# Kernel optimization log

Hardware: AMD Instinct MI355X
Metric: run time of the kernel (lower is better)

Reference implementation:

```python
import jax, jax.numpy as jnp
import numpy as np
from jax import lax

IMAGE_SIZE = 512
N_REWEIGHT = 3
BLUR_RADIUS = 4  # GaussianBlur(4)
BLUR_SIGMA = 4.0


def _cdist(a, b):
    # Euclidean distance matrix [N, M] via ||a||^2 + ||b||^2 - 2 a.b
    a2 = jnp.sum(a * a, axis=1)[:, None]
    b2 = jnp.sum(b * b, axis=1)[None, :]
    d2 = a2 + b2 - 2.0 * (a @ b.T)
    return jnp.sqrt(jnp.maximum(d2, 0.0))


def _gaussian_blur(img):
    # separable depthwise gaussian blur, kernel size 2*radius+1, SAME padding
    x = jnp.arange(-BLUR_RADIUS, BLUR_RADIUS + 1, dtype=img.dtype)
    g = jnp.exp(-(x * x) / (2.0 * BLUR_SIGMA * BLUR_SIGMA))
    g = g / jnp.sum(g)
    dn = ('NCHW', 'OIHW', 'NCHW')
    img = lax.conv_general_dilated(img, g.reshape(1, 1, -1, 1), (1, 1), 'SAME', dimension_numbers=dn)
    img = lax.conv_general_dilated(img, g.reshape(1, 1, 1, -1), (1, 1), 'SAME', dimension_numbers=dn)
    return img


def setup_inputs() -> dict:
    key = jax.random.key(0)
    k1, k2 = jax.random.split(key)
    h, w, d, m = 64, 64, 384, 65536
    patch = jax.random.normal(k1, (h * w, d), dtype=jnp.float32)
    patch_lib = jax.random.normal(k2, (m, d), dtype=jnp.float32)
    return {"patch": patch, "patch_lib": patch_lib, "fmap_h": h, "fmap_w": w}


def reference(patch, patch_lib, fmap_h, fmap_w):
    # dist: [N, M] full pairwise cdist against coreset library
    dist = _cdist(patch, patch_lib)
    min_val = jnp.min(dist, axis=1)            # [N] NN distance per test patch
    min_idx = jnp.argmin(dist, axis=1)         # [N]
    s_idx = jnp.argmax(min_val)
    s_star = jnp.max(min_val)
    m_test = patch[s_idx]                      # [D]
    m_star = patch_lib[min_idx[s_idx]]         # [D]
    # w_dist = cdist(m_star, patch_lib): single-row distance
    w_dist = jnp.sqrt(jnp.maximum(jnp.sum((m_star[None, :] - patch_lib) ** 2, axis=1), 0.0))
    neg_top, nn_idx = lax.top_k(-w_dist, N_REWEIGHT)   # k smallest
    m_star_knn = jnp.linalg.norm(m_test[None, :] - patch_lib[nn_idx[1:]], axis=1)  # [k-1]
    D = jnp.sqrt(jnp.asarray(patch.shape[1], dtype=patch.dtype))
    w = 1.0 - jnp.exp(s_star / D) / jnp.sum(jnp.exp(m_star_knn / D))
    s = w * s_star
    s_map = min_val.reshape(1, 1, fmap_h, fmap_w)
    s_map = jax.image.resize(s_map, (1, 1, IMAGE_SIZE, IMAGE_SIZE), method='bilinear')
    s_map = _gaussian_blur(s_map)
    return s, s_map
```

## Files before the change

### kernel.cpp

```cpp
#include <hip/hip_runtime.h>

#define NP 4096
#define DIM 384
#define ML 65536

typedef int i32x4 __attribute__((ext_vector_type(4)));
typedef unsigned short u16;
typedef unsigned long long u64;

#define QSCALE 21.16666667f
#define B2SCALE 224.0138889f
#define KBIAS (1 << 23)

typedef __attribute__((address_space(1))) unsigned int as1_u32;
typedef __attribute__((address_space(3))) unsigned int as3_u32;

__device__ __forceinline__ void gl_lds16(const void* g, void* l) {
  __builtin_amdgcn_global_load_lds((const as1_u32*)g, (as3_u32*)l, 16, 0, 0);
}

__global__ __launch_bounds__(256) void prep_kernel(const float* __restrict__ patch,
                                                   const float* __restrict__ lib,
                                                   char* __restrict__ Ai8,
                                                   char* __restrict__ Bi8,
                                                   int* __restrict__ b2i) {
  const int row = blockIdx.x * 4 + (threadIdx.x >> 6);
  const int lane = threadIdx.x & 63;
  const float* src;
  char* dst;
  int r;
  if (row < NP) { src = patch; dst = Ai8; r = row; }
  else          { src = lib;   dst = Bi8; r = row - NP; }
  float s = 0.f;
#pragma unroll
  for (int j = 0; j < 3; ++j) {
    const float2 v = *reinterpret_cast<const float2*>(src + (size_t)r * DIM + j * 128 + lane * 2);
    s += v.x * v.x + v.y * v.y;
    const int q0 = __float2int_rn(fminf(fmaxf(v.x, -6.f), 6.f) * QSCALE);
    const int q1 = __float2int_rn(fminf(fmaxf(v.y, -6.f), 6.f) * QSCALE);
    const u16 p = (u16)((q0 & 0xFF) | ((q1 & 0xFF) << 8));
    *reinterpret_cast<u16*>(dst + (size_t)r * DIM + j * 128 + lane * 2) = p;
  }
#pragma unroll
  for (int m = 1; m < 64; m <<= 1) s += __shfl_xor(s, m);
  if (lane == 0 && row >= NP) b2i[r] = __float2int_rn(s * B2SCALE);
}

__global__ __launch_bounds__(512, 2) void gemm_min_kernel(const char* __restrict__ Ai8,
                                                          const char* __restrict__ Bi8,
                                                          const int* __restrict__ b2i,
                                                          u64* __restrict__ packed) {
  __shared__ __align__(16) char As[2][32768];
  __shared__ __align__(16) char Bs[2][32768];
  const int tid = threadIdx.x;
  const int lane = tid & 63;
  const int w = tid >> 6;
  const int wm = w >> 2;
  const int wn = w & 3;
  const int cl = lane & 15, rg = lane >> 4;

  const int orig = blockIdx.x;
  const int logical = (orig & 7) * 512 + (orig >> 3);
  const int xt = logical & 15;
  const int yt = logical >> 4;
  const int n0 = xt * 256;
  const int m0 = yt * 256;

  const char* ga[4]; const char* gb[4]; int lof[4];
#pragma unroll
  for (int i = 0; i < 4; ++i) {
    const int P = i * 8192 + tid * 16;
    const int r = P >> 7;
    const int L = P ^ ((r & 7) << 4);
    const int c = L & 127;
    lof[i] = P;
    ga[i] = Ai8 + (size_t)(n0 + r) * DIM + c;
    gb[i] = Bi8 + (size_t)(m0 + r) * DIM + c;
  }

  int offA[2][8], offB[2][4];
#pragma unroll
  for (int g = 0; g < 2; ++g) {
#pragma unroll
    for (int j = 0; j < 8; ++j) {
      const int row = wm * 128 + j * 16 + cl;
      offA[g][j] = row * 128 + ((g * 64 + rg * 16) ^ ((cl & 7) << 4));
    }
#pragma unroll
    for (int i = 0; i < 4; ++i) {
      const int row = wn * 64 + i * 16 + cl;
      offB[g][i] = row * 128 + ((g * 64 + rg * 16) ^ ((cl & 7) << 4));
    }
  }

  i32x4 acc[4][8] = {};

#pragma unroll
  for (int i = 0; i < 4; ++i) { gl_lds16(ga[i], (char*)As[0] + lof[i]); ga[i] += 128; }
#pragma unroll
  for (int i = 0; i < 4; ++i) { gl_lds16(gb[i], (char*)Bs[0] + lof[i]); gb[i] += 128; }

#pragma unroll
  for (int kt = 0; kt < 3; ++kt) {
    const int buf = kt & 1;
    if (kt < 2) {
#pragma unroll
      for (int i = 0; i < 4; ++i) { gl_lds16(ga[i], (char*)As[buf ^ 1] + lof[i]); ga[i] += 128; }
#pragma unroll
      for (int i = 0; i < 4; ++i) { gl_lds16(gb[i], (char*)Bs[buf ^ 1] + lof[i]); gb[i] += 128; }
      asm volatile("s_waitcnt vmcnt(8)" ::: "memory");
    } else {
      asm volatile("s_waitcnt vmcnt(0)" ::: "memory");
    }
    __builtin_amdgcn_s_barrier();
    __builtin_amdgcn_sched_barrier(0);

    const char* Ab = (const char*)As[buf];
    const char* Bb = (const char*)Bs[buf];
#pragma unroll
    for (int g = 0; g < 2; ++g) {
      i32x4 af[8], bg[4];
#pragma unroll
      for (int j = 0; j < 8; ++j)
        af[j] = *reinterpret_cast<const i32x4*>(Ab + offA[g][j]);
#pragma unroll
      for (int i = 0; i < 4; ++i)
        bg[i] = *reinterpret_cast<const i32x4*>(Bb + offB[g][i]);
#pragma unroll
      for (int i = 0; i < 4; ++i)
#pragma unroll
        for (int j = 0; j < 8; ++j)
          acc[i][j] = __builtin_amdgcn_mfma_i32_16x16x64_i8(bg[i], af[j], acc[i][j], 0, 0, 0);
    }
    __builtin_amdgcn_s_barrier();
    __builtin_amdgcn_sched_barrier(0);
  }

  const int colb = m0 + wn * 64 + rg * 4;
  i32x4 bc[4];
#pragma unroll
  for (int i = 0; i < 4; ++i)
    bc[i] = *reinterpret_cast<const i32x4*>(&b2i[colb + i * 16]);

  u64* sh = reinterpret_cast<u64*>(As);

#pragma unroll
  for (int j = 0; j < 8; ++j) {
    const int prow = wm * 128 + j * 16 + cl;
    u64 best = ~0ull;
#pragma unroll
    for (int i = 0; i < 4; ++i)
#pragma unroll
      for (int r = 0; r < 4; ++r) {
        const unsigned kb = (unsigned)(bc[i][r] - acc[i][j][r] + KBIAS);
        const u64 p = ((u64)kb << 32) | (unsigned)(colb + i * 16 + r);
        best = p < best ? p : best;
      }
    const u64 o1 = __shfl_xor(best, 16); best = o1 < best ? o1 : best;
    const u64 o2 = __shfl_xor(best, 32); best = o2 < best ? o2 : best;
    if (rg == 0) sh[prow * 4 + wn] = best;
  }
  __syncthreads();
  if (tid < 256) {
    u64 v = sh[tid * 4];
#pragma unroll
    for (int k = 1; k < 4; ++k) { const u64 o = sh[tid * 4 + k]; v = o < v ? o : v; }
    atomicMin(&packed[n0 + tid], v);
  }
}

__global__ __launch_bounds__(256) void exactmin_kernel(const float* __restrict__ patch,
                                                       const float* __restrict__ lib,
                                                       u64* __restrict__ packed) {
  const int n = blockIdx.x * 4 + (threadIdx.x >> 6);
  const int lane = threadIdx.x & 63;
  const int idx = (int)(unsigned)packed[n];
  float s = 0.f;
#pragma unroll
  for (int j = 0; j < 3; ++j) {
    const float2 a = *reinterpret_cast<const float2*>(patch + (size_t)n * DIM + j * 128 + lane * 2);
    const float2 b = *reinterpret_cast<const float2*>(lib + (size_t)idx * DIM + j * 128 + lane * 2);
    const float d0 = a.x - b.x, d1 = a.y - b.y;
    s += d0 * d0 + d1 * d1;
  }
#pragma unroll
  for (int m = 1; m < 64; m <<= 1) s += __shfl_xor(s, m);
  if (lane == 0) packed[n] = ((u64)__float_as_uint(fmaxf(s, 0.f)) << 32) | (unsigned)idx;
}

__global__ __launch_bounds__(256) void cand_kernel(const u64* __restrict__ packed,
                                                   int* __restrict__ cand) {
  const int tid = threadIdx.x;
  float mx = -1.f;
  for (int n = tid; n < NP; n += 256) {
    const float v = __uint_as_float((unsigned)(packed[n] >> 32));
    mx = fmaxf(mx, v);
  }
#pragma unroll
  for (int m = 1; m < 64; m <<= 1) mx = fmaxf(mx, __shfl_xor(mx, m));
  __shared__ float wmax[4];
  __shared__ float smax;
  if ((tid & 63) == 0) wmax[tid >> 6] = mx;
  __syncthreads();
  if (tid == 0) {
    smax = fmaxf(fmaxf(wmax[0], wmax[1]), fmaxf(wmax[2], wmax[3]));
    cand[0] = 0;
  }
  __syncthreads();
  const float thr = smax - 8.0f;
  for (int n = tid; n < NP; n += 256) {
    const float v = __uint_as_float((unsigned)(packed[n] >> 32));
    if (v >= thr) {
      const int slot = atomicAdd(&cand[0], 1);
      if (slot < 256) cand[1 + slot] = n;
    }
  }
}

__global__ __launch_bounds__(256) void refine_kernel(const float* __restrict__ patch,
                                                     const float* __restrict__ lib,
                                                     const int* __restrict__ cand,
                                                     u64* __restrict__ refined) {
  const int cnt = min(cand[0], 256);
  const int tid = threadIdx.x, lane = tid & 63, w = tid >> 6;
  const int base = blockIdx.x * 32;
  __shared__ float a[8][DIM];
  __shared__ u64 rb[8][4];

  for (int g0 = 0; g0 < cnt; g0 += 8) {
    const int gc = min(cnt - g0, 8);
    for (int i = tid; i < gc * DIM; i += 256) {
      const int c = i / DIM, e = i - c * DIM;
      a[c][e] = patch[(size_t)cand[1 + g0 + c] * DIM + e];
    }
    __syncthreads();

    u64 wbest[8];
#pragma unroll
    for (int c = 0; c < 8; ++c) wbest[c] = ~0ull;

    for (int it = 0; it < 8; ++it) {
      const int m = base + w * 8 + it;
      float lr[6];
#pragma unroll
      for (int j = 0; j < 3; ++j) {
        const float2 v = *reinterpret_cast<const float2*>(lib + (size_t)m * DIM + j * 128 + lane * 2);
        lr[j * 2] = v.x; lr[j * 2 + 1] = v.y;
      }
#pragma unroll
      for (int c = 0; c < 8; ++c) {
        if (c >= gc) break;
        float s = 0.f;
#pragma unroll
        for (int j = 0; j < 3; ++j) {
          const float d0 = lr[j * 2] - a[c][j * 128 + lane * 2];
          const float d1 = lr[j * 2 + 1] - a[c][j * 128 + lane * 2 + 1];
          s += d0 * d0 + d1 * d1;
        }
#pragma unroll
        for (int msk = 1; msk < 64; msk <<= 1) s += __shfl_xor(s, msk);
        const u64 p = ((u64)__float_as_uint(s) << 32) | (unsigned)m;
        wbest[c] = p < wbest[c] ? p : wbest[c];
      }
    }
    if (lane == 0) {
#pragma unroll
      for (int c = 0; c < 8; ++c)
        if (c < gc) rb[c][w] = wbest[c];
    }
    __syncthreads();
    if (tid < gc) {
      u64 b = rb[tid][0];
#pragma unroll
      for (int k = 1; k < 4; ++k) b = rb[tid][k] < b ? rb[tid][k] : b;
      atomicMin(&refined[g0 + tid], b);
    }
    __syncthreads();
  }
}

__global__ __launch_bounds__(256) void pick_kernel(const u64* __restrict__ refined,
                                                   const int* __restrict__ cand,
                                                   int* __restrict__ scal_i,
                                                   float* __restrict__ scal_f) {
  const int tid = threadIdx.x, lane = tid & 63, w = tid >> 6;
  const int cnt = min(cand[0], 256);
  float v = -1.f;
  int nrow = 0x7FFFFFFF;
  int mi = 0;
  if (tid < cnt) {
    const u64 p = refined[tid];
    v = __uint_as_float((unsigned)(p >> 32));
    nrow = cand[1 + tid];
    mi = (int)(unsigned)p;
  }
#pragma unroll
  for (int msk = 1; msk < 64; msk <<= 1) {
    const float ov = __shfl_xor(v, msk);
    const int on = __shfl_xor(nrow, msk);
    const int om = __shfl_xor(mi, msk);
    if (ov > v || (ov == v && on < nrow)) { v = ov; nrow = on; mi = om; }
  }
  __shared__ float sv[4]; __shared__ int sn[4]; __shared__ int sm[4];
  if (lane == 0) { sv[w] = v; sn[w] = nrow; sm[w] = mi; }
  __syncthreads();
  if (tid == 0) {
    for (int k = 1; k < 4; ++k)
      if (sv[k] > v || (sv[k] == v && sn[k] < nrow)) { v = sv[k]; nrow = sn[k]; mi = sm[k]; }
    scal_i[0] = nrow;
    scal_i[1] = mi;
    scal_f[0] = sqrtf(fmaxf(v, 0.f));
  }
}

__device__ __forceinline__ void ins3u(u64 x, u64* v) {
  if (x < v[2]) {
    v[2] = x;
    if (v[2] < v[1]) { u64 t = v[1]; v[1] = v[2]; v[2] = t; }
    if (v[1] < v[0]) { u64 t = v[0]; v[0] = v[1]; v[1] = t; }
  }
}

__global__ __launch_bounds__(256) void wtop_kernel(const float* __restrict__ lib,
                                                   const int* __restrict__ scal_i,
                                                   u64* __restrict__ t3) {
  __shared__ float a[DIM];
  __shared__ u64 sv[12];
  const int tid = threadIdx.x, lane = tid & 63, w = tid >> 6;
  const int ms = scal_i[1];
  for (int i = tid; i < DIM; i += 256) a[i] = lib[(size_t)ms * DIM + i];
  __syncthreads();
  const int base = blockIdx.x * 32;
  u64 v[3] = {~0ull, ~0ull, ~0ull};
  for (int it = 0; it < 8; ++it) {
    const int m = base + w * 8 + it;
    float s = 0.f;
#pragma unroll
    for (int j = 0; j < 3; ++j) {
      const float2 lv = *reinterpret_cast<const float2*>(lib + (size_t)m * DIM + j * 128 + lane * 2);
      const float d0 = lv.x - a[j * 128 + lane * 2];
      const float d1 = lv.y - a[j * 128 + lane * 2 + 1];
      s += d0 * d0 + d1 * d1;
    }
#pragma unroll
    for (int msk = 1; msk < 64; msk <<= 1) s += __shfl_xor(s, msk);
    ins3u(((u64)__float_as_uint(s) << 32) | (unsigned)m, v);
  }
  if (lane == 0) {
#pragma unroll
    for (int k = 0; k < 3; ++k) sv[w * 3 + k] = v[k];
  }
  __syncthreads();
  if (tid == 0) {
    u64 fv[3] = {~0ull, ~0ull, ~0ull};
    for (int k = 0; k < 12; ++k) ins3u(sv[k], fv);
#pragma unroll
    for (int k = 0; k < 3; ++k) t3[blockIdx.x * 3 + k] = fv[k];
  }
}

__global__ __launch_bounds__(256) void final_kernel(const u64* __restrict__ t3,
                                                    const float* __restrict__ patch,
                                                    const float* __restrict__ lib,
                                                    const int* __restrict__ scal_i,
                                                    const float* __restrict__ scal_f,
                                                    float* __restrict__ out) {
  const int tid = threadIdx.x, lane = tid & 63, w = tid >> 6;
  u64 v[3] = {~0ull, ~0ull, ~0ull};
  for (int i = tid; i < 6144; i += 256) ins3u(t3[i], v);
#pragma unroll
  for (int msk = 1; msk < 64; msk <<= 1) {
    u64 o0 = __shfl_xor(v[0], msk);
    u64 o1 = __shfl_xor(v[1], msk);
    u64 o2 = __shfl_xor(v[2], msk);
    ins3u(o0, v); ins3u(o1, v); ins3u(o2, v);
  }
  __shared__ u64 sv[12];
  __shared__ int nn[2]; __shared__ float kk[2];
  if (lane == 0) {
#pragma unroll
    for (int k = 0; k < 3; ++k) sv[w * 3 + k] = v[k];
  }
  __syncthreads();
  if (tid == 0) {
    u64 fv[3] = {~0ull, ~0ull, ~0ull};
    for (int k = 0; k < 12; ++k) ins3u(sv[k], fv);
    nn[0] = (int)(unsigned)fv[1];
    nn[1] = (int)(unsigned)fv[2];
  }
  __syncthreads();
  if (w < 2) {
    const int s_idx = scal_i[0];
    const int nnx = nn[w];
    float s = 0.f;
#pragma unroll
    for (int k = 0; k < 6; ++k) {
      const float d = patch[(size_t)s_idx * DIM + lane + k * 64] - lib[(size_t)nnx * DIM + lane + k * 64];
      s += d * d;
    }
#pragma unroll
    for (int msk = 1; msk < 64; msk <<= 1) s += __shfl_xor(s, msk);
    if (lane == 0) kk[w] = sqrtf(s);
  }
  __syncthreads();
  if (tid == 0) {
    const float s_star = scal_f[0];
    const float Ds = 19.59591794f;
    const float wt = 1.0f - expf(s_star / Ds) / (expf(kk[0] / Ds) + expf(kk[1] / Ds));
    out[0] = wt * s_star;
  }
}

__device__ __constant__ float BW[9] = {
    0.0816741424f, 0.1016453893f, 0.1188358540f, 0.1305155396f, 0.1346581512f,
    0.1305155396f, 0.1188358540f, 0.1016453893f, 0.0816741424f};

__global__ __launch_bounds__(256) void scoremap_kernel(const u64* __restrict__ packed,
                                                       float* __restrict__ out) {
  __shared__ float mv[4096];
  __shared__ float t1b[12][512];
  __shared__ float t2b[4][512];
  const int tid = threadIdx.x;
  const int y0 = blockIdx.x * 4;

  for (int i = tid; i < 4096; i += 256)
    mv[i] = sqrtf(fmaxf(__uint_as_float((unsigned)(packed[i] >> 32)), 0.f));
  __syncthreads();

  for (int i = tid; i < 12 * 512; i += 256) {
    const int ry = i >> 9, x = i & 511;
    const int y = y0 - 4 + ry;
    float v = 0.f;
    if (y >= 0 && y < 512) {
      const float sy = y * 0.125f - 0.4375f;
      const float sx = x * 0.125f - 0.4375f;
      const int yy = (int)floorf(sy); const float fy = sy - (float)yy;
      const int xx = (int)floorf(sx); const float fx = sx - (float)xx;
      const int ya = max(yy, 0), yb = min(yy + 1, 63);
      const int xa = max(xx, 0), xb = min(xx + 1, 63);
      v = (1.f - fy) * ((1.f - fx) * mv[ya * 64 + xa] + fx * mv[ya * 64 + xb]) +
          fy * ((1.f - fx) * mv[yb * 64 + xa] + fx * mv[yb * 64 + xb]);
    }
    t1b[ry][x] = v;
  }
  __syncthreads();

  for (int i = tid; i < 4 * 512; i += 256) {
    const int r = i >> 9, x = i & 511;
    float s = 0.f;
#pragma unroll
    for (int k = -4; k <= 4; ++k) s += BW[k + 4] * t1b[r + 4 + k][x];
    t2b[r][x] = s;
  }
  __syncthreads();

  for (int i = tid; i < 4 * 512; i += 256) {
    const int r = i >> 9, x = i & 511;
    float s = 0.f;
#pragma unroll
    for (int k = -4; k <= 4; ++k) {
      const int xx = x + k;
      if (xx >= 0 && xx < 512) s += BW[k + 4] * t2b[r][xx];
    }
    out[(y0 + r) * 512 + x] = s;
  }
}

extern "C" void kernel_launch(void* const* d_in, const int* in_sizes, int n_in,
                              void* d_out, int out_size, void* d_ws, size_t ws_size,
                              hipStream_t stream) {
  const float* patch = (const float*)d_in[0];
  const float* lib = (const float*)d_in[1];
  float* out = (float*)d_out;

  char* ws = (char*)d_ws;
  size_t off = 0;
  auto alloc = [&](size_t bytes) {
    void* p = ws + off;
    off += (bytes + 255) & ~(size_t)255;
    return p;
  };
  char* Ai8 = (char*)alloc((size_t)NP * DIM);
  char* Bi8 = (char*)alloc((size_t)ML * DIM);
  int* b2i = (int*)alloc(ML * 4);
  u64* packed = (u64*)alloc(NP * 8);
  u64* refined = (u64*)alloc(256 * 8);
  int* cand = (int*)alloc(257 * 4);
  int* scal_i = (int*)alloc(64);
  float* scal_f = (float*)alloc(64);
  u64* t3 = (u64*)alloc(2048 * 3 * 8);

  hipMemsetAsync(packed, 0xFF, NP * 8, stream);
  hipMemsetAsync(refined, 0xFF, 256 * 8, stream);

  prep_kernel<<<(NP + ML) / 4, 256, 0, stream>>>(patch, lib, Ai8, Bi8, b2i);
  gemm_min_kernel<<<4096, 512, 0, stream>>>(Ai8, Bi8, b2i, packed);
  exactmin_kernel<<<NP / 4, 256, 0, stream>>>(patch, lib, packed);
  cand_kernel<<<1, 256, 0, stream>>>(packed, cand);
  refine_kernel<<<2048, 256, 0, stream>>>(patch, lib, cand, refined);
  pick_kernel<<<1, 256, 0, stream>>>(refined, cand, scal_i, scal_f);
  wtop_kernel<<<2048, 256, 0, stream>>>(lib, scal_i, t3);
  final_kernel<<<1, 256, 0, stream>>>(t3, patch, lib, scal_i, scal_f, out);
  scoremap_kernel<<<128, 256, 0, stream>>>(packed, out + 1);
}
```

Measured before the change: 260.3 us.

## Make GEMM-min kernel persistent over 16 library tiles with resident A panel

The int8 GEMM-min kernel now launches 256 persistent blocks instead of 4096. Each block keeps its full 256x384 A panel resident in LDS across three buffers and walks 16 consecutive 256-row library tiles. B k-slices are double-buffered, and each tile's epilogue overlaps the next tile's loads. Per-row minima are reduced with direct global atomicMin instead of through shared memory. This removes repeated A reloads and per-block launch and prologue overhead, at the cost of more LDS per block (lower occupancy) and more atomics.

After: 273.8 us. +5.2%, slower.

```diff
diff --git a/kernel.cpp b/kernel.cpp
--- a/kernel.cpp
+++ b/kernel.cpp
@@ -50,7 +50,7 @@
                                                           const char* __restrict__ Bi8,
                                                           const int* __restrict__ b2i,
                                                           u64* __restrict__ packed) {
-  __shared__ __align__(16) char As[2][32768];
+  __shared__ __align__(16) char As[3][32768];
   __shared__ __align__(16) char Bs[2][32768];
   const int tid = threadIdx.x;
   const int lane = tid & 63;
@@ -60,13 +60,14 @@
   const int cl = lane & 15, rg = lane >> 4;
 
   const int orig = blockIdx.x;
-  const int logical = (orig & 7) * 512 + (orig >> 3);
-  const int xt = logical & 15;
-  const int yt = logical >> 4;
-  const int n0 = xt * 256;
-  const int m0 = yt * 256;
-
-  const char* ga[4]; const char* gb[4]; int lof[4];
+  const int xcd = orig & 7;
+  const int local = orig >> 3;
+  const int nt = local & 15;
+  const int mg = xcd * 2 + (local >> 4);
+  const int n0 = nt * 256;
+  const int mbase = mg * 4096;
+
+  int lof[4]; const char* gaA[4]; const char* gbB[4];
 #pragma unroll
   for (int i = 0; i < 4; ++i) {
     const int P = i * 8192 + tid * 16;
@@ -74,8 +75,8 @@
     const int L = P ^ ((r & 7) << 4);
     const int c = L & 127;
     lof[i] = P;
-    ga[i] = Ai8 + (size_t)(n0 + r) * DIM + c;
-    gb[i] = Bi8 + (size_t)(m0 + r) * DIM + c;
+    gaA[i] = Ai8 + (size_t)(n0 + r) * DIM + c;
+    gbB[i] = Bi8 + (size_t)(mbase + r) * DIM + c;
   }
 
   int offA[2][8], offB[2][4];
@@ -94,79 +95,109 @@
   }
 
   i32x4 acc[4][8] = {};
-
-#pragma unroll
-  for (int i = 0; i < 4; ++i) { gl_lds16(ga[i], (char*)As[0] + lof[i]); ga[i] += 128; }
-#pragma unroll
-  for (int i = 0; i < 4; ++i) { gl_lds16(gb[i], (char*)Bs[0] + lof[i]); gb[i] += 128; }
-
-#pragma unroll
-  for (int kt = 0; kt < 3; ++kt) {
-    const int buf = kt & 1;
-    if (kt < 2) {
-#pragma unroll
-      for (int i = 0; i < 4; ++i) { gl_lds16(ga[i], (char*)As[buf ^ 1] + lof[i]); ga[i] += 128; }
-#pragma unroll
-      for (int i = 0; i < 4; ++i) { gl_lds16(gb[i], (char*)Bs[buf ^ 1] + lof[i]); gb[i] += 128; }
-      asm volatile("s_waitcnt vmcnt(8)" ::: "memory");
-    } else {
-      asm volatile("s_waitcnt vmcnt(0)" ::: "memory");
-    }
-    __builtin_amdgcn_s_barrier();
-    __builtin_amdgcn_sched_barrier(0);
-
-    const char* Ab = (const char*)As[buf];
-    const char* Bb = (const char*)Bs[buf];
-#pragma unroll
-    for (int g = 0; g < 2; ++g) {
-      i32x4 af[8], bg[4];
-#pragma unroll
-      for (int j = 0; j < 8; ++j)
-        af[j] = *reinterpret_cast<const i32x4*>(Ab + offA[g][j]);
-#pragma unroll
-      for (int i = 0; i < 4; ++i)
-        bg[i] = *reinterpret_cast<const i32x4*>(Bb + offB[g][i]);
-#pragma unroll
-      for (int i = 0; i < 4; ++i)
-#pragma unroll
-        for (int j = 0; j < 8; ++j)
-          acc[i][j] = __builtin_amdgcn_mfma_i32_16x16x64_i8(bg[i], af[j], acc[i][j], 0, 0, 0);
-    }
-    __builtin_amdgcn_s_barrier();
-    __builtin_amdgcn_sched_barrier(0);
-  }
-
-  const int colb = m0 + wn * 64 + rg * 4;
   i32x4 bc[4];
+
+#pragma unroll
+  for (int kt = 0; kt < 3; ++kt)
+#pragma unroll
+    for (int i = 0; i < 4; ++i)
+      gl_lds16(gaA[i] + kt * 128, (char*)As[kt] + lof[i]);
 #pragma unroll
   for (int i = 0; i < 4; ++i)
-    bc[i] = *reinterpret_cast<const i32x4*>(&b2i[colb + i * 16]);
-
-  u64* sh = reinterpret_cast<u64*>(As);
-
-#pragma unroll
-  for (int j = 0; j < 8; ++j) {
-    const int prow = wm * 128 + j * 16 + cl;
-    u64 best = ~0ull;
-#pragma unroll
-    for (int i = 0; i < 4; ++i)
-#pragma unroll
-      for (int r = 0; r < 4; ++r) {
-        const unsigned kb = (unsigned)(bc[i][r] - acc[i][j][r] + KBIAS);
-        const u64 p = ((u64)kb << 32) | (unsigned)(colb + i * 16 + r);
-        best = p < best ? p : best;
-      }
-    const u64 o1 = __shfl_xor(best, 16); best = o1 < best ? o1 : best;
-    const u64 o2 = __shfl_xor(best, 32); best = o2 < best ? o2 : best;
-    if (rg == 0) sh[prow * 4 + wn] = best;
-  }
-  __syncthreads();
-  if (tid < 256) {
-    u64 v = sh[tid * 4];
-#pragma unroll
-    for (int k = 1; k < 4; ++k) { const u64 o = sh[tid * 4 + k]; v = o < v ? o : v; }
-    atomicMin(&packed[n0 + tid], v);
-  }
+    gl_lds16(gbB[i], (char*)Bs[0] + lof[i]);
+
+#define STAGE_B(MT, KT, BUF)                                                        \
+  {                                                                                 \
+    _Pragma("unroll")                                                               \
+    for (int i = 0; i < 4; ++i)                                                     \
+      gl_lds16(gbB[i] + (size_t)(MT) * 98304 + (KT) * 128, (char*)Bs[BUF] + lof[i]); \
+  }
+
+#define MFMA_STEP(KT, BUF)                                                          \
+  {                                                                                 \
+    const char* Ab = (const char*)As[KT];                                           \
+    const char* Bb = (const char*)Bs[BUF];                                          \
+    _Pragma("unroll")                                                               \
+    for (int g = 0; g < 2; ++g) {                                                   \
+      i32x4 af[8], bg[4];                                                           \
+      _Pragma("unroll")                                                             \
+      for (int j = 0; j < 8; ++j) af[j] = *reinterpret_cast<const i32x4*>(Ab + offA[g][j]); \
+      _Pragma("unroll")                                                             \
+      for (int i = 0; i < 4; ++i) bg[i] = *reinterpret_cast<const i32x4*>(Bb + offB[g][i]); \
+      _Pragma("unroll")                                                             \
+      for (int i = 0; i < 4; ++i)                                                   \
+        _Pragma("unroll")                                                           \
+        for (int j = 0; j < 8; ++j)                                                 \
+          acc[i][j] = __builtin_amdgcn_mfma_i32_16x16x64_i8(bg[i], af[j], acc[i][j], 0, 0, 0); \
+    }                                                                               \
+  }
+
+#define EPILOGUE(M0V)                                                               \
+  {                                                                                 \
+    const int colb = (M0V) + wn * 64 + rg * 4;                                      \
+    _Pragma("unroll")                                                               \
+    for (int j = 0; j < 8; ++j) {                                                   \
+      const int prow = wm * 128 + j * 16 + cl;                                      \
+      u64 best = ~0ull;                                                             \
+      _Pragma("unroll")                                                             \
+      for (int i = 0; i < 4; ++i)                                                   \
+        _Pragma("unroll")                                                           \
+        for (int r = 0; r < 4; ++r) {                                               \
+          const unsigned kb = (unsigned)(bc[i][r] - acc[i][j][r] + KBIAS);          \
+          const u64 p = ((u64)kb << 32) | (unsigned)(colb + i * 16 + r);            \
+          best = p < best ? p : best;                                               \
+        }                                                                           \
+      const u64 o1 = __shfl_xor(best, 16); best = o1 < best ? o1 : best;            \
+      const u64 o2 = __shfl_xor(best, 32); best = o2 < best ? o2 : best;            \
+      if (rg == 0) atomicMin(&packed[n0 + prow], best);                             \
+    }                                                                               \
+    _Pragma("unroll")                                                               \
+    for (int i = 0; i < 4; ++i)                                                     \
+      _Pragma("unroll")                                                             \
+      for (int j = 0; j < 8; ++j) acc[i][j] = i32x4{0, 0, 0, 0};                    \
+  }
+
+#define WAITV(N) asm volatile("s_waitcnt vmcnt(" #N ")" ::: "memory")
+#define BARRIER() { __builtin_amdgcn_s_barrier(); __builtin_amdgcn_sched_barrier(0); }
+
+#define TILE_BODY(MT, BUF0, FIRST, LAST)                                            \
+  {                                                                                 \
+    const int m0v = mbase + (MT) * 256;                                             \
+    if (!(FIRST)) { EPILOGUE(m0v - 256); }                                          \
+    STAGE_B(MT, 1, (BUF0) ^ 1);                                                     \
+    _Pragma("unroll")                                                               \
+    for (int i = 0; i < 4; ++i)                                                     \
+      bc[i] = *reinterpret_cast<const i32x4*>(&b2i[m0v + wn * 64 + rg * 4 + i * 16]); \
+    if (FIRST) { WAITV(8); } else { WAITV(16); }                                    \
+    BARRIER();                                                                      \
+    MFMA_STEP(0, (BUF0));                                                           \
+    BARRIER();                                                                      \
+    STAGE_B(MT, 2, (BUF0));                                                         \
+    WAITV(8);                                                                       \
+    BARRIER();                                                                      \
+    MFMA_STEP(1, (BUF0) ^ 1);                                                       \
+    BARRIER();                                                                      \
+    if (!(LAST)) { STAGE_B((MT) + 1, 0, (BUF0) ^ 1); WAITV(4); }                    \
+    else         { WAITV(0); }                                                      \
+    BARRIER();                                                                      \
+    MFMA_STEP(2, (BUF0));                                                           \
+    BARRIER();                                                                      \
+  }
+
+#pragma unroll 1
+  for (int mt2 = 0; mt2 < 8; ++mt2) {
+    const int mtA = mt2 * 2;
+    TILE_BODY(mtA, 0, (mtA == 0), false);
+    TILE_BODY(mtA + 1, 1, false, (mtA + 1 == 15));
+  }
+  EPILOGUE(mbase + 15 * 256);
+
+#undef TILE_BODY
+#undef WAITV
+#undef BARRIER
+#undef EPILOGUE
+#undef MFMA_STEP
+#undef STAGE_B
 }
 
 __global__ __launch_bounds__(256) void exactmin_kernel(const float* __restrict__ patch,
@@ -494,7 +525,7 @@
   hipMemsetAsync(refined, 0xFF, 256 * 8, stream);
 
   prep_kernel<<<(NP + ML) / 4, 256, 0, stream>>>(patch, lib, Ai8, Bi8, b2i);
-  gemm_min_kernel<<<4096, 512, 0, stream>>>(Ai8, Bi8, b2i, packed);
+  gemm_min_kernel<<<256, 512, 0, stream>>>(Ai8, Bi8, b2i, packed);
   exactmin_kernel<<<NP / 4, 256, 0, stream>>>(patch, lib, packed);
   cand_kernel<<<1, 256, 0, stream>>>(packed, cand);
   refine_kernel<<<2048, 256, 0, stream>>>(patch, lib, cand, refined);
```
